# Kernel tuning notes

Measured on AMD Instinct MI355X. Metric: run time of the kernel, lower is better.

Reference implementation:

```python
import jax, jax.numpy as jnp
import numpy as np

B = 2; L = 64; HOP = 256; T = L * HOP
IN_CH = 101; INNER = 128; COND = 81
NBLOCK = 2; LAYERS = 5; K = 3; KH = 64
COUT = 2 * INNER
KCH = INNER * COUT * K * LAYERS   # 491520
BCH = COUT * LAYERS               # 1280


def setup_inputs() -> dict:
    key = jax.random.key(0)
    ks = jax.random.split(key, 12)
    n = lambda k, s, sc: jax.random.normal(k, s, jnp.float32) * sc
    return {
        "x": n(ks[0], (B, IN_CH, T), 1.0),
        "c": n(ks[1], (B, COND, L), 1.0),
        "fc_W": n(ks[2], (INNER, IN_CH), 0.1),
        "fc_b": jnp.zeros((INNER,), jnp.float32),
        "inp_W": n(ks[3], (NBLOCK, KH, COND, 5), 0.05),
        "inp_b": jnp.zeros((NBLOCK, KH), jnp.float32),
        "res1_W": n(ks[4], (NBLOCK, KH, KH), 0.1),
        "res1_b": jnp.zeros((NBLOCK, KH), jnp.float32),
        "res2_W": n(ks[5], (NBLOCK, KH, KH), 0.1),
        "res2_b": jnp.zeros((NBLOCK, KH), jnp.float32),
        "kern_W": n(ks[6], (NBLOCK, KCH, KH), 0.02),
        "kern_b": jnp.zeros((NBLOCK, KCH), jnp.float32),
        "biasc_W": n(ks[7], (NBLOCK, BCH, KH), 0.02),
        "biasc_b": jnp.zeros((NBLOCK, BCH), jnp.float32),
        "lc1_W": n(ks[8], (INNER, INNER), 0.08),
        "lc1_b": jnp.zeros((INNER,), jnp.float32),
        "lc2_W": n(ks[9], (1, INNER), 0.08),
        "lc2_b": jnp.zeros((1,), jnp.float32),
    }


def _conv1x1(x, W, b):
    return jnp.einsum('oc,bcl->bol', W, x) + b[None, :, None]


def _conv5(x, W, b):
    y = jax.lax.conv_general_dilated(x, W, (1,), [(2, 2)],
                                     dimension_numbers=('NCH', 'OIH', 'NCH'))
    return y + b[None, :, None]


def _lrelu(x):
    return jnp.where(x >= 0, x, 0.1 * x)


def _kernel_predictor(c, iW, ib, r1W, r1b, r2W, r2b, kW, kb, bW, bb):
    h = _lrelu(_conv5(c, iW, ib))
    h = h + _conv1x1(_lrelu(_conv1x1(h, r1W, r1b)), r2W, r2b)
    k = _conv1x1(h, kW, kb)   # (B, KCH, L)
    bb_ = _conv1x1(h, bW, bb)  # (B, BCH, L)
    Bn, _, Ln = c.shape
    kernels = k.reshape(Bn, LAYERS, INNER, COUT, K, Ln)
    bias = bb_.reshape(Bn, LAYERS, COUT, Ln)
    return kernels, bias


def _lvc(x, kernel, bias, dilation, hop):
    # x: (B, Cin, T); kernel: (B, Cin, Cout, K, L); bias: (B, Cout, L)
    Bn, Cin, Tn = x.shape
    _, _, O, Kn, Ln = kernel.shape
    p = dilation * (Kn - 1) // 2
    xp = jnp.pad(x, ((0, 0), (0, 0), (p, p)))
    win = hop + 2 * p
    # per-window gather (unfold over time with stride hop)
    idx = (jnp.arange(Ln) * hop)[:, None] + jnp.arange(win)[None, :]
    xw = xp[:, :, idx]
    m = win // dilation                                  # hop/d + (K-1)
    xt = xw.reshape(Bn, Cin, Ln, m, dilation).transpose(0, 1, 2, 4, 3)  # (B,Cin,L,d,m)
    S = hop // dilation
    idx2 = jnp.arange(S)[:, None] + jnp.arange(Kn)[None, :]  # (S, K) sliding taps
    xu = xt[..., idx2]                                   # (B, Cin, L, d, S, K)
    o = jnp.einsum('bildsk,biokl->bolsd', xu, kernel)
    o = o + bias[:, :, :, None, None]
    return o.reshape(Bn, O, Tn)


def _lvc_block(x, c, iW, ib, r1W, r1b, r2W, r2b, kW, kb, bW, bb):
    kernels, bias = _kernel_predictor(c, iW, ib, r1W, r1b, r2W, r2b, kW, kb, bW, bb)
    for i in range(LAYERS):
        d = 2 ** i  # max 16 < hop, so hop<dilation branch never triggers
        y = _lvc(x, kernels[:, i], bias[:, i], d, HOP)
        x = jax.nn.sigmoid(y[:, :INNER]) * jnp.tanh(y[:, INNER:])
    return x


def reference(x, c, fc_W, fc_b, inp_W, inp_b, res1_W, res1_b, res2_W, res2_b,
              kern_W, kern_b, biasc_W, biasc_b, lc1_W, lc1_b, lc2_W, lc2_b):
    h = _conv1x1(x, fc_W, fc_b)
    for n_ in range(NBLOCK):
        y = _lvc_block(h, c, inp_W[n_], inp_b[n_], res1_W[n_], res1_b[n_],
                       res2_W[n_], res2_b[n_], kern_W[n_], kern_b[n_],
                       biasc_W[n_], biasc_b[n_])
        h = y if n_ == 0 else h + y
    h = jnp.maximum(h, 0.0)
    h = _conv1x1(h, lc1_W, lc1_b)
    h = jnp.maximum(h, 0.0)
    h = _conv1x1(h, lc2_W, lc2_b)
    return h
```

## Files before the change

kernel.cpp:

```cpp
#include <hip/hip_runtime.h>
#include <math.h>

#define BB     2
#define LSEG   64
#define HOP    256
#define TT     (LSEG*HOP)
#define IN_CH  101
#define INNER  128
#define COND   81
#define LAYERS 5
#define KTAP   3
#define KH     64
#define COUT   256
#define RPL    (INNER*COUT*KTAP)
#define KCH    (RPL*LAYERS)
#define BCH    (COUT*LAYERS)
#define NBL    (BB*LSEG)
#define XS     36
#define AS_STR 72
#define CS_STR 136

typedef _Float16 f16;
typedef _Float16 f16x2 __attribute__((ext_vector_type(2)));
typedef _Float16 f16x4 __attribute__((ext_vector_type(4)));
typedef _Float16 f16x8 __attribute__((ext_vector_type(8)));
typedef float    f32x4 __attribute__((ext_vector_type(4)));

__global__ __launch_bounds__(256) void k_fc(const float* __restrict__ x,
                                            const float* __restrict__ W,
                                            const float* __restrict__ bias,
                                            f16* __restrict__ out) {
    int half = blockIdx.x & 1;
    int g = (blockIdx.x >> 1)*256 + threadIdx.x;
    int b = g / TT, t = g % TT;
    float xv[IN_CH];
    const float* xp = x + (size_t)b*IN_CH*TT + t;
#pragma unroll
    for (int c = 0; c < IN_CH; ++c) xv[c] = xp[(size_t)c*TT];
    f16* op = out + (size_t)b*INNER*TT + t;
    int o0 = half*64;
    for (int o = o0; o < o0 + 64; ++o) {
        const float* wr = W + o*IN_CH;
        float a0 = bias[o], a1 = 0.f, a2 = 0.f, a3 = 0.f;
#pragma unroll
        for (int c = 0; c + 3 < IN_CH; c += 4) {
            a0 += wr[c]*xv[c]; a1 += wr[c+1]*xv[c+1];
            a2 += wr[c+2]*xv[c+2]; a3 += wr[c+3]*xv[c+3];
        }
        a0 += wr[100]*xv[100];
        op[(size_t)o*TT] = (f16)((a0+a1)+(a2+a3));
    }
}

__global__ __launch_bounds__(256) void k_h1(const float* __restrict__ cc,
                                            const float* __restrict__ iW,
                                            const float* __restrict__ ib,
                                            float* __restrict__ h1buf) {
    int og = blockIdx.x & 7;
    int bp = blockIdx.x >> 3;
    int b  = bp & 1;
    int n  = bp >> 1;
    __shared__ float cL[COND*LSEG];
    __shared__ float wL[8*COND*5];
    int tid = threadIdx.x;
    for (int idx = tid; idx < COND*LSEG; idx += 256)
        cL[idx] = cc[(size_t)b*COND*LSEG + idx];
    const float* wsrc = iW + (size_t)n*KH*COND*5 + (size_t)og*8*COND*5;
    for (int idx = tid; idx < 8*COND*5; idx += 256)
        wL[idx] = wsrc[idx];
    __syncthreads();
#pragma unroll
    for (int rep = 0; rep < 2; ++rep) {
        int idx = rep*256 + tid;
        int ol = idx >> 6, l = idx & 63;
        int o  = og*8 + ol;
        float acc = ib[n*KH + o];
        const float* wrow = wL + ol*COND*5;
        for (int i = 0; i < COND; ++i) {
            const float* crow = cL + i*LSEG;
            const float* w5 = wrow + i*5;
#pragma unroll
            for (int k = 0; k < 5; ++k) {
                int ll = l + k - 2;
                if (ll >= 0 && ll < LSEG) acc += crow[ll]*w5[k];
            }
        }
        h1buf[(((size_t)(n*BB + b))*KH + o)*LSEG + l] = acc >= 0.f ? acc : 0.1f*acc;
    }
}

__global__ __launch_bounds__(256) void k_h2t(const float* __restrict__ h1buf,
                                             const float* __restrict__ r1W,
                                             const float* __restrict__ r1b,
                                             const float* __restrict__ r2W,
                                             const float* __restrict__ r2b,
                                             float* __restrict__ h2buf,
                                             f16* __restrict__ h2h) {
    int b = blockIdx.x & 1;
    int n = blockIdx.x >> 1;
    __shared__ float h1L[KH*LSEG];
    __shared__ float t1L[KH*LSEG];
    __shared__ float wL[KH*KH];
    int tid = threadIdx.x;
    const float* h1src = h1buf + ((size_t)(n*BB + b))*KH*LSEG;
    for (int idx = tid; idx < KH*LSEG; idx += 256)
        h1L[idx] = h1src[idx];
    for (int idx = tid; idx < KH*KH; idx += 256)
        wL[idx] = r1W[(size_t)n*KH*KH + idx];
    __syncthreads();
#pragma unroll
    for (int rep = 0; rep < 16; ++rep) {
        int idx = rep*256 + tid;
        int o = idx >> 6, l = idx & 63;
        float acc = r1b[n*KH + o];
        const float* wr = wL + o*KH;
#pragma unroll
        for (int i = 0; i < KH; ++i) acc += wr[i]*h1L[i*LSEG + l];
        t1L[idx] = acc >= 0.f ? acc : 0.1f*acc;
    }
    __syncthreads();
    for (int idx = tid; idx < KH*KH; idx += 256)
        wL[idx] = r2W[(size_t)n*KH*KH + idx];
    __syncthreads();
#pragma unroll
    for (int rep = 0; rep < 16; ++rep) {
        int idx = rep*256 + tid;
        int o = idx >> 6, l = idx & 63;
        float acc = r2b[n*KH + o];
        const float* wr = wL + o*KH;
#pragma unroll
        for (int i = 0; i < KH; ++i) acc += wr[i]*t1L[i*LSEG + l];
        float h2 = h1L[o*LSEG + l] + acc;
        size_t row = (size_t)n*NBL + b*LSEG + l;
        h2buf[row*KH + o] = h2;
        h2h  [row*KH + o] = (f16)h2;
    }
}

__global__ __launch_bounds__(256) void k_biash(const float* __restrict__ bW,
                                               const float* __restrict__ bb,
                                               const float* __restrict__ h2buf,
                                               float* __restrict__ biasbuf) {
    int tg = blockIdx.x*256 + threadIdx.x;
    int n  = __builtin_amdgcn_readfirstlane(tg / (BB*BCH));
    int rem = tg - n*(BB*BCH);
    int b  = __builtin_amdgcn_readfirstlane(rem / BCH);
    int rb = rem % BCH;
    float w[KH];
    const float4* wp = (const float4*)(bW + ((size_t)n*BCH + rb)*KH);
#pragma unroll
    for (int q = 0; q < KH/4; ++q) {
        float4 v = wp[q];
        w[4*q] = v.x; w[4*q+1] = v.y; w[4*q+2] = v.z; w[4*q+3] = v.w;
    }
    float bv = bb[n*BCH + rb];
    for (int l = 0; l < LSEG; ++l) {
        size_t row = (size_t)n*NBL + b*LSEG + l;
        const float* h2 = h2buf + row*KH;
        float a0 = bv, a1 = 0.f, a2 = 0.f, a3 = 0.f;
#pragma unroll
        for (int j = 0; j < KH; j += 4) {
            a0 += w[j]*h2[j]; a1 += w[j+1]*h2[j+1];
            a2 += w[j+2]*h2[j+2]; a3 += w[j+3]*h2[j+3];
        }
        biasbuf[row*BCH + rb] = (a0+a1)+(a2+a3);
    }
}

__global__ __launch_bounds__(256) void k_gen(const float* __restrict__ kW,
                                             const float* __restrict__ kb,
                                             const f16*   __restrict__ h2h,
                                             f16*         __restrict__ kbuf) {
    int o   = blockIdx.x & 255;
    int tmp = blockIdx.x >> 8;
    int tap = tmp % 3;  tmp /= 3;
    int lay = tmp % 5;
    int n   = tmp / 5;
    int tid  = threadIdx.x;
    int lane = tid & 63;
    int wm   = tid >> 6;
    int n16  = lane & 15;
    int quad = lane >> 4;

    __shared__ f16 smem[128*CS_STR];
    __shared__ float biasL[128];

    size_t rbase = (size_t)n*KCH + (size_t)lay*RPL;
    const f16* h2b = h2h + (size_t)n*NBL*KH;

#pragma unroll
    for (int it = 0; it < 8; ++it) {
        int g = it*256 + tid;
        int c = g >> 4, f4i = g & 15;
        const float4* arow = (const float4*)(kW + (rbase + (size_t)(c*COUT + o)*KTAP + tap)*KH);
        float4 v = arow[f4i];
        *(f16x4*)&smem[c*AS_STR + f4i*4] = f16x4{(f16)v.x,(f16)v.y,(f16)v.z,(f16)v.w};
    }
    if (tid < 128)
        biasL[tid] = kb[rbase + (size_t)(tid*COUT + o)*KTAP + tap];
    __syncthreads();

    f16x8 afr[2][2];
    f32x4 bini[2];
#pragma unroll
    for (int j = 0; j < 2; ++j) {
        int c = wm*32 + j*16 + n16;
#pragma unroll
        for (int ks = 0; ks < 2; ++ks)
            afr[j][ks] = *(const f16x8*)&smem[c*AS_STR + ks*32 + quad*8];
#pragma unroll
        for (int r = 0; r < 4; ++r)
            bini[j][r] = biasL[wm*32 + j*16 + quad*4 + r];
    }
    __syncthreads();

#pragma unroll 2
    for (int t = 0; t < 8; ++t) {
        int bl = t*16 + n16;
        const f16* brow = h2b + (size_t)bl*KH;
        f16x8 bf0 = *(const f16x8*)(brow + quad*8);
        f16x8 bf1 = *(const f16x8*)(brow + 32 + quad*8);
        f32x4 acc0 = bini[0], acc1 = bini[1];
        acc0 = __builtin_amdgcn_mfma_f32_16x16x32_f16(afr[0][0], bf0, acc0, 0, 0, 0);
        acc0 = __builtin_amdgcn_mfma_f32_16x16x32_f16(afr[0][1], bf1, acc0, 0, 0, 0);
        acc1 = __builtin_amdgcn_mfma_f32_16x16x32_f16(afr[1][0], bf0, acc1, 0, 0, 0);
        acc1 = __builtin_amdgcn_mfma_f32_16x16x32_f16(afr[1][1], bf1, acc1, 0, 0, 0);
        int c0 = wm*32 + quad*4;
        *(f16x4*)&smem[bl*CS_STR + c0] =
            f16x4{(f16)acc0[0],(f16)acc0[1],(f16)acc0[2],(f16)acc0[3]};
        *(f16x4*)&smem[bl*CS_STR + c0 + 16] =
            f16x4{(f16)acc1[0],(f16)acc1[1],(f16)acc1[2],(f16)acc1[3]};
    }
    __syncthreads();

    int op = (o < 128) ? 2*o : 2*(o-128) + 1;
    f16* kout = kbuf + ((size_t)(n*LAYERS + lay)*NBL)*RPL + (size_t)op*384 + (size_t)tap*128;
#pragma unroll
    for (int it = 0; it < 8; ++it) {
        int g = it*256 + tid;
        int row = g >> 4, seg = g & 15;
        *(f16x8*)(kout + (size_t)row*RPL + seg*8) = *(const f16x8*)&smem[row*CS_STR + seg*8];
    }
}

template<int DIL>
__global__ __launch_bounds__(512) void k_lvc(const f16* __restrict__ xin,
                                             const f16* __restrict__ kbuf,
                                             const float* __restrict__ biasbuf,
                                             f16* __restrict__ xout,
                                             int layerIdx) {
    constexpr int WIN = 256 + 2*DIL;
    int wg  = blockIdx.x;
    int o0  = (wg & 3)*64;
    int l   = (wg >> 2) & 63;
    int b   = wg >> 8;
    int bl  = b*LSEG + l;
    int tid = threadIdx.x;
    int w   = tid >> 6;
    int lane = tid & 63;
    int quad = lane >> 4;
    int n16  = lane & 15;
    int wo = (w & 1)*32;
    int wt = (w >> 1)*64;

    __shared__ f16 As[3*64*XS];
    __shared__ f16 xwin[288*XS];

    const float* bias_l = biasbuf + (size_t)bl*BCH + layerIdx*COUT;
    f32x4 acc[2][4];
#pragma unroll
    for (int j = 0; j < 2; ++j) {
        int g0 = (o0 + wo + j*16 + quad*4) >> 1;
        f32x4 ini;
        ini[0] = bias_l[g0];       ini[1] = bias_l[g0 + 128];
        ini[2] = bias_l[g0 + 1];   ini[3] = bias_l[g0 + 1 + 128];
#pragma unroll
        for (int tt = 0; tt < 4; ++tt) acc[j][tt] = ini;
    }

    const f16* xb = xin + (size_t)b*INNER*TT;
    const f16* kbl = kbuf + (size_t)bl*RPL + (size_t)o0*384;
    int o_l = (tid & 255) >> 2, q4 = tid & 3;
    int gt0 = l*256 - DIL;

    for (int cb = 0; cb < 4; ++cb) {
        for (int cc = w; cc < 32; cc += 8) {
            const f16* src = xb + (size_t)(cb*32 + cc)*TT;
#pragma unroll
            for (int tw0 = 0; tw0 < WIN; tw0 += 64) {
                int tw = tw0 + lane;
                if (tw < WIN) {
                    int gt = gt0 + tw;
                    f16 v = ((unsigned)gt < (unsigned)TT) ? src[gt] : (f16)0.f;
                    xwin[tw*XS + cc] = v;
                }
            }
        }
        if (tid < 256) {
#pragma unroll
            for (int tap = 0; tap < 3; ++tap) {
                f16x8 v = *(const f16x8*)&kbl[(size_t)o_l*384 + tap*128 + cb*32 + q4*8];
                *(f16x8*)&As[(tap*64 + o_l)*XS + q4*8] = v;
            }
        }
        __syncthreads();
#pragma unroll
        for (int tap = 0; tap < 3; ++tap) {
            f16x8 af0 = *(const f16x8*)&As[(tap*64 + wo + n16)*XS + quad*8];
            f16x8 af1 = *(const f16x8*)&As[(tap*64 + wo + 16 + n16)*XS + quad*8];
#pragma unroll
            for (int tt = 0; tt < 4; ++tt) {
                int trow = wt + tt*16 + n16 + tap*DIL;
                f16x8 bf = *(const f16x8*)&xwin[trow*XS + quad*8];
                acc[0][tt] = __builtin_amdgcn_mfma_f32_16x16x32_f16(af0, bf, acc[0][tt], 0, 0, 0);
                acc[1][tt] = __builtin_amdgcn_mfma_f32_16x16x32_f16(af1, bf, acc[1][tt], 0, 0, 0);
            }
        }
        __syncthreads();
    }
    f16* ob = xout + (size_t)b*INNER*TT + l*256;
#pragma unroll
    for (int j = 0; j < 2; ++j) {
        int g0 = (o0 + wo + j*16 + quad*4) >> 1;
#pragma unroll
        for (int tt = 0; tt < 4; ++tt) {
            int tloc = wt + tt*16 + n16;
            f32x4 a = acc[j][tt];
            float s0  = 1.f/(1.f + __expf(-a[0]));
            float th0 = 2.f/(1.f + __expf(-2.f*a[1])) - 1.f;
            float s1  = 1.f/(1.f + __expf(-a[2]));
            float th1 = 2.f/(1.f + __expf(-2.f*a[3])) - 1.f;
            ob[(size_t)g0*TT + tloc]     = (f16)(s0*th0);
            ob[(size_t)(g0+1)*TT + tloc] = (f16)(s1*th1);
        }
    }
}

__global__ __launch_bounds__(256) void k_head(const f16* __restrict__ y0,
                                              const f16* __restrict__ y1,
                                              const float* __restrict__ W1,
                                              const float* __restrict__ b1,
                                              const float* __restrict__ W2,
                                              const float* __restrict__ b2,
                                              float* __restrict__ out) {
    int b    = blockIdx.x >> 8;
    int tseg = (blockIdx.x & 255)*64;
    int tid  = threadIdx.x;
    int w    = tid >> 6;
    int lane = tid & 63;
    int t    = tseg + lane;
    __shared__ float red[4][64];

    float h[INNER];
    const f16* p0 = y0 + (size_t)b*INNER*TT + t;
    const f16* p1 = y1 + (size_t)b*INNER*TT + t;
#pragma unroll
    for (int c = 0; c < INNER; ++c) {
        float v = (float)p0[(size_t)c*TT] + (float)p1[(size_t)c*TT];
        h[c] = v > 0.f ? v : 0.f;
    }
    float part = 0.f;
    int oBase = w*32;
    for (int oi = 0; oi < 32; ++oi) {
        int o = oBase + oi;
        const float* wr = W1 + o*INNER;
        float z0 = b1[o], z1 = 0.f, z2 = 0.f, z3 = 0.f;
#pragma unroll
        for (int c = 0; c < INNER; c += 4) {
            z0 += wr[c]*h[c];   z1 += wr[c+1]*h[c+1];
            z2 += wr[c+2]*h[c+2]; z3 += wr[c+3]*h[c+3];
        }
        float z = (z0+z1)+(z2+z3);
        z = z > 0.f ? z : 0.f;
        part += W2[o]*z;
    }
    red[w][lane] = part;
    __syncthreads();
    if (w == 0) {
        float acc = b2[0] + red[0][lane] + red[1][lane] + red[2][lane] + red[3][lane];
        out[(size_t)b*TT + t] = acc;
    }
}

extern "C" void kernel_launch(void* const* d_in, const int* in_sizes, int n_in,
                              void* d_out, int out_size, void* d_ws, size_t ws_size,
                              hipStream_t stream) {
    const float* x    = (const float*)d_in[0];
    const float* c    = (const float*)d_in[1];
    const float* fcW  = (const float*)d_in[2];
    const float* fcb  = (const float*)d_in[3];
    const float* inpW = (const float*)d_in[4];
    const float* inpb = (const float*)d_in[5];
    const float* r1W  = (const float*)d_in[6];
    const float* r1b  = (const float*)d_in[7];
    const float* r2W  = (const float*)d_in[8];
    const float* r2b  = (const float*)d_in[9];
    const float* kW   = (const float*)d_in[10];
    const float* kb   = (const float*)d_in[11];
    const float* bW   = (const float*)d_in[12];
    const float* bb   = (const float*)d_in[13];
    const float* l1W  = (const float*)d_in[14];
    const float* l1b  = (const float*)d_in[15];
    const float* l2W  = (const float*)d_in[16];
    const float* l2b  = (const float*)d_in[17];

    float* ws = (float*)d_ws;
    float* h2buf   = ws;
    float* biasbuf = h2buf + (size_t)2*NBL*KH;
    float* h1buf   = biasbuf + (size_t)2*NBL*BCH;
    f16*   h2h     = (f16*)(h1buf + (size_t)2*BB*KH*LSEG);
    f16*   bufA    = h2h + (size_t)2*NBL*KH;
    f16*   bufB    = bufA + (size_t)BB*INNER*TT;
    f16*   bufC    = bufB + (size_t)BB*INNER*TT;
    f16*   kbuf    = bufC + (size_t)BB*INNER*TT;

    k_fc<<<BB*TT/256*2, 256, 0, stream>>>(x, fcW, fcb, bufA);

    k_h1<<<32, 256, 0, stream>>>(c, inpW, inpb, h1buf);
    k_h2t<<<4, 256, 0, stream>>>(h1buf, r1W, r1b, r2W, r2b, h2buf, h2h);
    k_biash<<<20, 256, 0, stream>>>(bW, bb, h2buf, biasbuf);
    k_gen<<<2*LAYERS*3*256, 256, 0, stream>>>(kW, kb, h2h, kbuf);

    for (int n = 0; n < 2; ++n) {
        const float* bias_n = biasbuf + (size_t)n*NBL*BCH;
        f16* pin = (n == 0) ? bufA : bufB;
        f16* s0  = (n == 0) ? bufB : bufC;
        f16* s1  = (n == 0) ? bufC : bufA;
        f16* cin = pin;
        for (int i = 0; i < LAYERS; ++i) {
            const f16* kslice = kbuf + (size_t)(n*LAYERS + i)*NBL*RPL;
            f16* cout_ = (i % 2 == 0) ? s0 : s1;
            switch (i) {
                case 0: k_lvc<1> <<<BB*LSEG*4, 512, 0, stream>>>(cin, kslice, bias_n, cout_, i); break;
                case 1: k_lvc<2> <<<BB*LSEG*4, 512, 0, stream>>>(cin, kslice, bias_n, cout_, i); break;
                case 2: k_lvc<4> <<<BB*LSEG*4, 512, 0, stream>>>(cin, kslice, bias_n, cout_, i); break;
                case 3: k_lvc<8> <<<BB*LSEG*4, 512, 0, stream>>>(cin, kslice, bias_n, cout_, i); break;
                case 4: k_lvc<16><<<BB*LSEG*4, 512, 0, stream>>>(cin, kslice, bias_n, cout_, i); break;
            }
            cin = cout_;
        }
    }
    k_head<<<BB*TT/64, 256, 0, stream>>>(bufB, bufC, l1W, l1b, l2W, l2b, (float*)d_out);
}
```

Before: 1.009 ms.

## Store activations time-major and feed LVC MFMA B-operands directly from global

Activations change from channel-major (B,C,T) to time-major (B,T,C) f16 in the fc, LVC and head kernels. The fc and LVC kernels stage outputs in shared memory and write coalesced 16-byte vectors. The LVC kernel no longer builds a transposed x window in LDS per channel block. It loads all three taps' kernel weights once and reads B fragments as contiguous 8-half vectors from global memory with a bounds check. This removes scalar strided gathers and most barriers, but B-operand reads now depend on L1/L2 hits and re-read overlapping rows across taps.

```diff
diff --git a/kernel.cpp b/kernel.cpp
--- a/kernel.cpp
+++ b/kernel.cpp
@@ -16,9 +16,11 @@
 #define KCH    (RPL*LAYERS)
 #define BCH    (COUT*LAYERS)
 #define NBL    (BB*LSEG)
-#define XS     36
 #define AS_STR 72
 #define CS_STR 136
+#define AK_STR 136
+#define TS_STR 34
+
 
 typedef _Float16 f16;
 typedef _Float16 f16x2 __attribute__((ext_vector_type(2)));
@@ -33,22 +35,31 @@
     int half = blockIdx.x & 1;
     int g = (blockIdx.x >> 1)*256 + threadIdx.x;
     int b = g / TT, t = g % TT;
+    int tseg = t - (int)threadIdx.x;
+    __shared__ f16 T[256*(64+2)];
     float xv[IN_CH];
     const float* xp = x + (size_t)b*IN_CH*TT + t;
 #pragma unroll
     for (int c = 0; c < IN_CH; ++c) xv[c] = xp[(size_t)c*TT];
-    f16* op = out + (size_t)b*INNER*TT + t;
     int o0 = half*64;
-    for (int o = o0; o < o0 + 64; ++o) {
-        const float* wr = W + o*IN_CH;
-        float a0 = bias[o], a1 = 0.f, a2 = 0.f, a3 = 0.f;
+    for (int oi = 0; oi < 64; ++oi) {
+        const float* wr = W + (o0 + oi)*IN_CH;
+        float a0 = bias[o0 + oi], a1 = 0.f, a2 = 0.f, a3 = 0.f;
 #pragma unroll
         for (int c = 0; c + 3 < IN_CH; c += 4) {
             a0 += wr[c]*xv[c]; a1 += wr[c+1]*xv[c+1];
             a2 += wr[c+2]*xv[c+2]; a3 += wr[c+3]*xv[c+3];
         }
         a0 += wr[100]*xv[100];
-        op[(size_t)o*TT] = (f16)((a0+a1)+(a2+a3));
+        T[threadIdx.x*66 + oi] = (f16)((a0+a1)+(a2+a3));
+    }
+    __syncthreads();
+    f16* ob = out + ((size_t)b*TT + tseg)*INNER + o0;
+#pragma unroll
+    for (int it = 0; it < 8; ++it) {
+        int idx = it*256 + threadIdx.x;
+        int row = idx >> 3, seg = idx & 7;
+        *(f16x8*)(ob + (size_t)row*INNER + seg*8) = *(const f16x8*)&T[row*66 + seg*8];
     }
 }
 
@@ -249,7 +260,6 @@
                                              const float* __restrict__ biasbuf,
                                              f16* __restrict__ xout,
                                              int layerIdx) {
-    constexpr int WIN = 256 + 2*DIL;
     int wg  = blockIdx.x;
     int o0  = (wg & 3)*64;
     int l   = (wg >> 2) & 63;
@@ -263,8 +273,8 @@
     int wo = (w & 1)*32;
     int wt = (w >> 1)*64;
 
-    __shared__ f16 As[3*64*XS];
-    __shared__ f16 xwin[288*XS];
+    __shared__ f16 As[3*64*AK_STR];
+    f16* Ttile = As;
 
     const float* bias_l = biasbuf + (size_t)bl*BCH + layerIdx*COUT;
     f32x4 acc[2][4];
@@ -278,50 +288,46 @@
         for (int tt = 0; tt < 4; ++tt) acc[j][tt] = ini;
     }
 
-    const f16* xb = xin + (size_t)b*INNER*TT;
+    const f16* xb  = xin + (size_t)b*TT*INNER;
     const f16* kbl = kbuf + (size_t)bl*RPL + (size_t)o0*384;
-    int o_l = (tid & 255) >> 2, q4 = tid & 3;
-    int gt0 = l*256 - DIL;
-
-    for (int cb = 0; cb < 4; ++cb) {
-        for (int cc = w; cc < 32; cc += 8) {
-            const f16* src = xb + (size_t)(cb*32 + cc)*TT;
-#pragma unroll
-            for (int tw0 = 0; tw0 < WIN; tw0 += 64) {
-                int tw = tw0 + lane;
-                if (tw < WIN) {
-                    int gt = gt0 + tw;
-                    f16 v = ((unsigned)gt < (unsigned)TT) ? src[gt] : (f16)0.f;
-                    xwin[tw*XS + cc] = v;
-                }
-            }
-        }
-        if (tid < 256) {
-#pragma unroll
-            for (int tap = 0; tap < 3; ++tap) {
-                f16x8 v = *(const f16x8*)&kbl[(size_t)o_l*384 + tap*128 + cb*32 + q4*8];
-                *(f16x8*)&As[(tap*64 + o_l)*XS + q4*8] = v;
-            }
-        }
-        __syncthreads();
-#pragma unroll
-        for (int tap = 0; tap < 3; ++tap) {
-            f16x8 af0 = *(const f16x8*)&As[(tap*64 + wo + n16)*XS + quad*8];
-            f16x8 af1 = *(const f16x8*)&As[(tap*64 + wo + 16 + n16)*XS + quad*8];
+
+#pragma unroll
+    for (int it = 0; it < 6; ++it) {
+        int idx = it*512 + tid;
+        int row = idx / 48;
+        int s   = idx - row*48;
+        int tap = s >> 4, ks = s & 15;
+        f16x8 v = *(const f16x8*)&kbl[(size_t)row*384 + s*8];
+        *(f16x8*)&As[(tap*64 + row)*AK_STR + ks*8] = v;
+    }
+    __syncthreads();
+
+    int tbase = l*256 + wt + n16 - DIL;
+#pragma unroll
+    for (int tap = 0; tap < 3; ++tap) {
+        const f16* arow0 = &As[(tap*64 + wo + n16)*AK_STR];
+        const f16* arow1 = &As[(tap*64 + wo + 16 + n16)*AK_STR];
+#pragma unroll
+        for (int kc = 0; kc < 4; ++kc) {
+            f16x8 af0 = *(const f16x8*)(arow0 + kc*32 + quad*8);
+            f16x8 af1 = *(const f16x8*)(arow1 + kc*32 + quad*8);
 #pragma unroll
             for (int tt = 0; tt < 4; ++tt) {
-                int trow = wt + tt*16 + n16 + tap*DIL;
-                f16x8 bf = *(const f16x8*)&xwin[trow*XS + quad*8];
+                int gt = tbase + tt*16 + tap*DIL;
+                f16x8 bf = f16x8{(f16)0,(f16)0,(f16)0,(f16)0,(f16)0,(f16)0,(f16)0,(f16)0};
+                if ((unsigned)gt < (unsigned)TT)
+                    bf = *(const f16x8*)(xb + (size_t)gt*INNER + kc*32 + quad*8);
                 acc[0][tt] = __builtin_amdgcn_mfma_f32_16x16x32_f16(af0, bf, acc[0][tt], 0, 0, 0);
                 acc[1][tt] = __builtin_amdgcn_mfma_f32_16x16x32_f16(af1, bf, acc[1][tt], 0, 0, 0);
             }
         }
-        __syncthreads();
-    }
-    f16* ob = xout + (size_t)b*INNER*TT + l*256;
+    }
+    __syncthreads();
+
 #pragma unroll
     for (int j = 0; j < 2; ++j) {
         int g0 = (o0 + wo + j*16 + quad*4) >> 1;
+        int cl = g0 - (o0 >> 1);
 #pragma unroll
         for (int tt = 0; tt < 4; ++tt) {
             int tloc = wt + tt*16 + n16;
@@ -330,9 +336,16 @@
             float th0 = 2.f/(1.f + __expf(-2.f*a[1])) - 1.f;
             float s1  = 1.f/(1.f + __expf(-a[2]));
             float th1 = 2.f/(1.f + __expf(-2.f*a[3])) - 1.f;
-            ob[(size_t)g0*TT + tloc]     = (f16)(s0*th0);
-            ob[(size_t)(g0+1)*TT + tloc] = (f16)(s1*th1);
-        }
+            *(f16x2*)&Ttile[tloc*TS_STR + cl] = f16x2{(f16)(s0*th0), (f16)(s1*th1)};
+        }
+    }
+    __syncthreads();
+    f16* ob = xout + ((size_t)b*TT + l*256)*INNER + (o0 >> 1);
+#pragma unroll
+    for (int it = 0; it < 2; ++it) {
+        int idx = it*512 + tid;
+        int row = idx >> 2, seg = idx & 3;
+        *(f16x8*)(ob + (size_t)row*INNER + seg*8) = *(const f16x8*)&Ttile[row*TS_STR + seg*8];
     }
 }
 
@@ -352,12 +365,17 @@
     __shared__ float red[4][64];
 
     float h[INNER];
-    const f16* p0 = y0 + (size_t)b*INNER*TT + t;
-    const f16* p1 = y1 + (size_t)b*INNER*TT + t;
-#pragma unroll
-    for (int c = 0; c < INNER; ++c) {
-        float v = (float)p0[(size_t)c*TT] + (float)p1[(size_t)c*TT];
-        h[c] = v > 0.f ? v : 0.f;
+    const f16* p0 = y0 + ((size_t)b*TT + t)*INNER;
+    const f16* p1 = y1 + ((size_t)b*TT + t)*INNER;
+#pragma unroll
+    for (int q = 0; q < 16; ++q) {
+        f16x8 a  = *(const f16x8*)(p0 + q*8);
+        f16x8 bq = *(const f16x8*)(p1 + q*8);
+#pragma unroll
+        for (int j = 0; j < 8; ++j) {
+            float v = (float)a[j] + (float)bq[j];
+            h[q*8 + j] = v > 0.f ? v : 0.f;
+        }
     }
     float part = 0.f;
     int oBase = w*32;
```

Measured after the change: 1.106 ms. 1.1x slower.
